# Kernel tuning notes

Hardware: AMD Instinct MI355X
Metric: run time of the kernel (lower is better)

The kernel has to match this reference:

```python
import jax, jax.numpy as jnp
import numpy as np

D_MODEL = 256
N_HEADS = 8
D_FF = 1024
N_LAYERS = 6
INPUT_DIM = 2
EPS = 1e-5  # torch LayerNorm default


def _layer_norm(x, g, b):
    m = jnp.mean(x, axis=-1, keepdims=True)
    v = jnp.mean((x - m) ** 2, axis=-1, keepdims=True)
    return (x - m) / jnp.sqrt(v + EPS) * g + b


def setup_inputs() -> dict:
    key = jax.random.key(0)
    ks = jax.random.split(key, 8)
    f32 = jnp.float32

    def w(k, shape, fan_in):
        return jax.random.normal(k, shape, f32) * (1.0 / np.sqrt(fan_in))

    return {
        "x": jax.random.normal(ks[0], (8, 1024, INPUT_DIM), f32),
        "in_w": w(ks[1], (INPUT_DIM, D_MODEL), INPUT_DIM),
        "in_b": jnp.zeros((D_MODEL,), f32),
        "ln1_g": jnp.ones((D_MODEL,), f32),
        "ln1_b": jnp.zeros((D_MODEL,), f32),
        "qkv_w": w(ks[2], (D_MODEL, 3 * D_MODEL), D_MODEL),
        "qkv_b": jnp.zeros((3 * D_MODEL,), f32),
        "out_w": w(ks[3], (D_MODEL, D_MODEL), D_MODEL),
        "out_b": jnp.zeros((D_MODEL,), f32),
        "lna_g": jnp.ones((D_MODEL,), f32),
        "lna_b": jnp.zeros((D_MODEL,), f32),
        "ln2_g": jnp.ones((D_MODEL,), f32),
        "ln2_b": jnp.zeros((D_MODEL,), f32),
        "ff1_w": w(ks[4], (D_MODEL, D_FF), D_MODEL),
        "ff1_b": jnp.zeros((D_FF,), f32),
        "ff2_w": w(ks[5], (D_FF, D_MODEL), D_FF),
        "ff2_b": jnp.zeros((D_MODEL,), f32),
        "lnf_g": jnp.ones((D_MODEL,), f32),
        "lnf_b": jnp.zeros((D_MODEL,), f32),
    }


def reference(x, in_w, in_b, ln1_g, ln1_b, qkv_w, qkv_b, out_w, out_b,
              lna_g, lna_b, ln2_g, ln2_b, ff1_w, ff1_b, ff2_w, ff2_b,
              lnf_g, lnf_b):
    B, L, _ = x.shape
    dk = D_MODEL // N_HEADS
    scale = 1.0 / np.sqrt(dk)
    top_k = max(1, L // 4)

    # sinusoidal positional encoding [L, D]
    pos = jnp.arange(L, dtype=jnp.float32)[:, None]
    div = jnp.exp(jnp.arange(0, D_MODEL, 2, dtype=jnp.float32)
                  * (-np.log(10000.0) / D_MODEL))
    pe = jnp.zeros((L, D_MODEL), jnp.float32)
    pe = pe.at[:, 0::2].set(jnp.sin(pos * div))
    pe = pe.at[:, 1::2].set(jnp.cos(pos * div))

    h = x @ in_w + in_b + pe[None]  # [B, L, D]

    # VoformerEncoder reuses the SAME layer object -> shared weights, 6 passes
    for _ in range(N_LAYERS):
        # --- self-attention sublayer (pre-norm) ---
        s2 = _layer_norm(h, ln1_g, ln1_b)
        qkv = (s2 @ qkv_w + qkv_b).reshape(B, L, 3, N_HEADS, dk)
        q = qkv[:, :, 0].transpose(0, 2, 1, 3)  # [B, H, L, dk]
        k = qkv[:, :, 1].transpose(0, 2, 1, 3)
        v = qkv[:, :, 2].transpose(0, 2, 1, 3)

        scores = jnp.einsum('bhqd,bhkd->bhqk', q, k) * scale  # [B,H,L,L]
        # ProbSparse: keep only the per-row top-k scores
        thr = jax.lax.top_k(scores, top_k)[0][..., -1:]
        sparse = jnp.where(scores >= thr, scores, -jnp.inf)
        attn = jax.nn.softmax(sparse, axis=-1)
        o = jnp.einsum('bhqk,bhkd->bhqd', attn, v)
        o = o.transpose(0, 2, 1, 3).reshape(B, L, D_MODEL)
        o = o @ out_w + out_b
        # InformerAttention applies its own residual + LayerNorm
        attn_out = _layer_norm(o + s2, lna_g, lna_b)
        h = h + attn_out

        # --- FFN sublayer with Volatilite activation ---
        s2 = _layer_norm(h, ln2_g, ln2_b)
        f = s2 @ ff1_w + ff1_b  # [B, L, d_ff]
        mean_f = jnp.mean(f, axis=1, keepdims=True)
        vol = jnp.sqrt(jnp.mean((mean_f - f) ** 2, axis=1, keepdims=True))
        f = f * vol
        f = f @ ff2_w + ff2_b
        h = h + f

    return _layer_norm(h, lnf_g, lnf_b)
```

## Files before the change

### kernel.cpp

```cpp
#include <hip/hip_runtime.h>
#include <hip/hip_bf16.h>
#include <math.h>

#define D_MODEL 256
#define NH 8
#define DFF 1024
#define NLAYERS 6
#define B_ 8
#define L_ 1024
#define NR (B_*L_)
#define TOPK 256
#define LNEPS 1e-5f

typedef __attribute__((ext_vector_type(8))) short bf16x8;
typedef __attribute__((ext_vector_type(4))) float f32x4;

__device__ __forceinline__ float wsum(float v){
  #pragma unroll
  for(int o=32;o>0;o>>=1) v += __shfl_xor(v,o,64);
  return v;
}
__device__ __forceinline__ short f2bf(float x){
  unsigned u = __float_as_uint(x);
  u += 0x7fffu + ((u>>16)&1u);
  return (short)(u>>16);
}
__device__ __forceinline__ float bf2f(short s){
  return __uint_as_float(((unsigned)(unsigned short)s)<<16);
}
__device__ __forceinline__ unsigned pk2bf(float a, float b){
  __hip_bfloat162 h = __float22bfloat162_rn(make_float2(a,b));
  unsigned u; __builtin_memcpy(&u, &h, 4);
  return u;
}
__device__ __forceinline__ float kinvf(int k){
  unsigned u = (k & 0x8000) ? ((unsigned)k ^ 0x8000u) : ((unsigned)k ^ 0xFFFFu);
  return __uint_as_float(u << 16);
}
__device__ __forceinline__ void g2l(const short* g, short* l){
  __builtin_amdgcn_global_load_lds(
      (const __attribute__((address_space(1))) unsigned int*)g,
      (__attribute__((address_space(3))) unsigned int*)l,
      16, 0, 0);
}

__global__ __launch_bounds__(256) void embed_kernel(
    const float* __restrict__ x, const float* __restrict__ in_w,
    const float* __restrict__ in_b, float* __restrict__ h)
{
  int tid = blockIdx.x*256 + threadIdx.x;
  int n  = tid >> 6;
  int d0 = (tid & 63) << 2;
  int l  = n & (L_-1);
  float x0 = x[2*n], x1 = x[2*n+1];
  const float kf = -0.07195578415606394f;
  float pe[4];
  #pragma unroll
  for(int ii=0; ii<2; ++ii){
    int i = (d0>>1) + ii;
    float dv  = expf((float)i * kf);
    float ang = (float)l * dv;
    pe[2*ii]   = sinf(ang);
    pe[2*ii+1] = cosf(ang);
  }
  float4 w0 = *(const float4*)(in_w + d0);
  float4 w1 = *(const float4*)(in_w + D_MODEL + d0);
  float4 bb = *(const float4*)(in_b + d0);
  float4 o;
  o.x = x0*w0.x + x1*w1.x + bb.x + pe[0];
  o.y = x0*w0.y + x1*w1.y + bb.y + pe[1];
  o.z = x0*w0.z + x1*w1.z + bb.z + pe[2];
  o.w = x0*w0.w + x1*w1.w + bb.w + pe[3];
  *(float4*)(h + (size_t)n*D_MODEL + d0) = o;
}

__global__ __launch_bounds__(256) void wcvt(
    const float* __restrict__ W, short* __restrict__ WT, int N, int kshift)
{
  int idx = blockIdx.x*256 + threadIdx.x;
  int K = 1<<kshift;
  if (idx >= N*K) return;
  int n = idx >> kshift, k = idx & (K-1);
  WT[idx] = f2bf(W[(size_t)k*N + n]);
}

template<int OM>
__global__ __launch_bounds__(256) void ln_kernel(
    const float* __restrict__ in, const float* __restrict__ g,
    const float* __restrict__ b, float* __restrict__ out,
    short* __restrict__ outb)
{
  int wave = threadIdx.x >> 6, lane = threadIdx.x & 63;
  int row = blockIdx.x*4 + wave;
  float4 v = ((const float4*)(in + (size_t)row*D_MODEL))[lane];
  float s  = v.x+v.y+v.z+v.w;
  float sq = v.x*v.x+v.y*v.y+v.z*v.z+v.w*v.w;
  s = wsum(s); sq = wsum(sq);
  float mean = s*(1.f/D_MODEL);
  float var  = sq*(1.f/D_MODEL) - mean*mean;
  float rstd = 1.f/sqrtf(var + LNEPS);
  float4 gv = ((const float4*)g)[lane];
  float4 bv = ((const float4*)b)[lane];
  float4 o;
  o.x = (v.x-mean)*rstd*gv.x + bv.x;
  o.y = (v.y-mean)*rstd*gv.y + bv.y;
  o.z = (v.z-mean)*rstd*gv.z + bv.z;
  o.w = (v.w-mean)*rstd*gv.w + bv.w;
  if (OM == 0){
    ((float4*)(out + (size_t)row*D_MODEL))[lane] = o;
  }
  if (OM == 2){
    uint2 pk; pk.x = pk2bf(o.x, o.y); pk.y = pk2bf(o.z, o.w);
    *(uint2*)(outb + (size_t)row*D_MODEL + lane*4) = pk;
  }
}

__global__ __launch_bounds__(256) void lnln_kernel(
    const float* __restrict__ tb,
    const float* __restrict__ ga, const float* __restrict__ ba,
    const float* __restrict__ g2, const float* __restrict__ b2,
    float* __restrict__ h, short* __restrict__ s2b)
{
  int wave = threadIdx.x >> 6, lane = threadIdx.x & 63;
  int row = blockIdx.x*4 + wave;
  float4 v = ((const float4*)(tb + (size_t)row*D_MODEL))[lane];
  float s  = v.x+v.y+v.z+v.w;
  float sq = v.x*v.x+v.y*v.y+v.z*v.z+v.w*v.w;
  s = wsum(s); sq = wsum(sq);
  float mean = s*(1.f/D_MODEL);
  float var  = sq*(1.f/D_MODEL) - mean*mean;
  float rstd = 1.f/sqrtf(var + LNEPS);
  float4 gv = ((const float4*)ga)[lane];
  float4 bv = ((const float4*)ba)[lane];
  float4* hp = (float4*)(h + (size_t)row*D_MODEL) + lane;
  float4 hv = *hp;
  float4 hn;
  hn.x = hv.x + (v.x-mean)*rstd*gv.x + bv.x;
  hn.y = hv.y + (v.y-mean)*rstd*gv.y + bv.y;
  hn.z = hv.z + (v.z-mean)*rstd*gv.z + bv.z;
  hn.w = hv.w + (v.w-mean)*rstd*gv.w + bv.w;
  *hp = hn;
  float s2  = hn.x+hn.y+hn.z+hn.w;
  float sq2 = hn.x*hn.x+hn.y*hn.y+hn.z*hn.z+hn.w*hn.w;
  s2 = wsum(s2); sq2 = wsum(sq2);
  float m2 = s2*(1.f/D_MODEL);
  float v2 = sq2*(1.f/D_MODEL) - m2*m2;
  float r2 = 1.f/sqrtf(v2 + LNEPS);
  float4 g2v = ((const float4*)g2)[lane];
  float4 b2v = ((const float4*)b2)[lane];
  uint2 pk;
  pk.x = pk2bf((hn.x-m2)*r2*g2v.x + b2v.x, (hn.y-m2)*r2*g2v.y + b2v.y);
  pk.y = pk2bf((hn.z-m2)*r2*g2v.z + b2v.z, (hn.w-m2)*r2*g2v.w + b2v.w);
  *(uint2*)(s2b + (size_t)row*D_MODEL + lane*4) = pk;
}

template<int MODE>
__global__ __launch_bounds__(256) void mfma_gemm(
    const short* __restrict__ A, const short* __restrict__ BT,
    const float* __restrict__ bias, const short* __restrict__ residb,
    float* __restrict__ Cf, short* __restrict__ Cb, short* __restrict__ Vt,
    int N, int K)
{
  __shared__ __align__(16) short As[128*32];
  __shared__ __align__(16) short Bs[64*32];
  const int t = threadIdx.x, wv = t>>6, lane = t&63;
  const int r16 = lane&15, quad = lane>>4;
  const int m0 = blockIdx.y*128, n0 = blockIdx.x*64;
  const int ia0 = wv*128 + lane, ia1 = ia0 + 64;
  const int ib  = wv*64 + lane;
  const short* Ab = A  + (size_t)m0*K;
  const short* Bb = BT + (size_t)n0*K;
  const f32x4 z = {0.f,0.f,0.f,0.f};
  f32x4 acc[2][4];
  #pragma unroll
  for (int i=0;i<2;++i)
    #pragma unroll
    for (int j=0;j<4;++j) acc[i][j] = z;

  for (int k0 = 0; k0 < K; k0 += 32){
    __syncthreads();
    g2l(Ab + (size_t)(ia0>>2)*K + k0 + (ia0&3)*8, As + ia0*8);
    g2l(Ab + (size_t)(ia1>>2)*K + k0 + (ia1&3)*8, As + ia1*8);
    g2l(Bb + (size_t)(ib>>2)*K  + k0 + (ib&3)*8,  Bs + ib*8);
    __syncthreads();
    bf16x8 af0 = *(const bf16x8*)(As + ((wv*32      + r16)*32 + quad*8));
    bf16x8 af1 = *(const bf16x8*)(As + ((wv*32 + 16 + r16)*32 + quad*8));
    bf16x8 bf[4];
    #pragma unroll
    for (int ct=0; ct<4; ++ct)
      bf[ct] = *(const bf16x8*)(Bs + ((ct*16 + r16)*32 + quad*8));
    #pragma unroll
    for (int ct=0; ct<4; ++ct){
      acc[0][ct] = __builtin_amdgcn_mfma_f32_16x16x32_bf16(af0, bf[ct], acc[0][ct], 0,0,0);
      acc[1][ct] = __builtin_amdgcn_mfma_f32_16x16x32_bf16(af1, bf[ct], acc[1][ct], 0,0,0);
    }
  }

  #pragma unroll
  for (int rt=0; rt<2; ++rt){
    const int mb = m0 + wv*32 + rt*16 + quad*4;
    #pragma unroll
    for (int ct=0; ct<4; ++ct){
      const int n = n0 + ct*16 + r16;
      const float bv = bias[n];
      if (MODE == 0){
        if (n < 512){
          int region = n>>8, hh = (n>>5)&7, d = n&31;
          #pragma unroll
          for (int r=0;r<4;++r){
            int l = mb + r;
            size_t base = (((size_t)(region*64 + (l>>10)*8 + hh))*1024 + (l&1023))*32 + d;
            Cb[base] = f2bf(acc[rt][ct][r] + bv);
          }
        } else {
          int dv = n - 512, hh = dv>>5, d = dv&31;
          int b = mb>>10, lloc = mb&1023;
          size_t base = (((size_t)(b*8 + hh))*32 + d)*1024 + lloc;
          uint2 pk;
          pk.x = pk2bf(acc[rt][ct][0] + bv, acc[rt][ct][1] + bv);
          pk.y = pk2bf(acc[rt][ct][2] + bv, acc[rt][ct][3] + bv);
          *(uint2*)(Vt + base) = pk;
        }
      } else {
        #pragma unroll
        for (int r=0;r<4;++r){
          size_t off = (size_t)(mb + r)*N + n;
          float c = acc[rt][ct][r] + bv;
          if (MODE == 1) Cf[off] = c + bf2f(residb[off]);
          if (MODE == 2) Cb[off] = f2bf(c);
          if (MODE == 3) Cf[off] += c;
        }
      }
    }
  }
}

__global__ __launch_bounds__(512,8) void attn_mfma(
    const short* __restrict__ qkbf, const short* __restrict__ vT,
    short* __restrict__ ob)
{
  __shared__ __align__(16) short sc16[16*1024];
  __shared__ __align__(16) float po[8*256];
  const int t = threadIdx.x, wv = t>>6, lane = t&63;
  const int r16 = lane&15, quad = lane>>4;
  const int blk = blockIdx.x;
  const int bh = (blk & 7)*8 + ((blk>>3)&7);
  const int qt = blk >> 6;

  bf16x8 aq = *(const bf16x8*)(qkbf + ((size_t)bh*1024 + qt*16 + r16)*32 + quad*8);
  const short* kb = qkbf + (size_t)(64 + bh)*1024*32;
  short* p0 = sc16 + quad*4096;

  #pragma unroll
  for (int g=0; g<2; ++g){
    bf16x8 bkb[4];
    #pragma unroll
    for (int j=0;j<4;++j)
      bkb[j] = *(const bf16x8*)(kb + (size_t)(wv*128 + (g*4+j)*16 + r16)*32 + quad*8);
    #pragma unroll
    for (int j=0;j<4;++j){
      f32x4 c = {0.f,0.f,0.f,0.f};
      c = __builtin_amdgcn_mfma_f32_16x16x32_bf16(aq, bkb[j], c, 0, 0, 0);
      const int keyq = (wv*128 + (g*4+j)*16 + r16) ^ ((quad&1)<<5);
      unsigned u01 = pk2bf(c[0], c[1]);
      unsigned u23 = pk2bf(c[2], c[3]);
      p0[keyq]               = (short)u01;
      p0[1024 + (keyq ^ 8)]  = (short)(u01>>16);
      p0[2048 + (keyq ^ 16)] = (short)u23;
      p0[3072 + (keyq ^ 24)] = (short)(u23>>16);
    }
  }
  __syncthreads();

  const float SC2 = 0.25500529485087056f;
  {
    const int ra = wv*2;
    const int sa = (ra&7)<<3;
    short* pa = sc16 + ra*1024 + ((2*lane) ^ sa);
    short* pb = sc16 + (ra+1)*1024 + (((2*lane) ^ sa) ^ 8);
    float fa[16], fb[16];
    #pragma unroll
    for (int i=0;i<8;++i){
      unsigned wa = *(const unsigned*)(pa + i*128);
      unsigned wb = *(const unsigned*)(pb + i*128);
      fa[2*i]   = __uint_as_float(wa << 16);
      fa[2*i+1] = __uint_as_float(wa & 0xFFFF0000u);
      fb[2*i]   = __uint_as_float(wb << 16);
      fb[2*i+1] = __uint_as_float(wb & 0xFFFF0000u);
    }
    int loA = 0, loB = 0;
    #pragma unroll
    for (int bit = 15; bit >= 0; --bit){
      const int mA = loA | (1<<bit);
      const int mB = loB | (1<<bit);
      const float tA = kinvf(mA);
      const float tB = kinvf(mB);
      int cA = 0, cB = 0;
      #pragma unroll
      for (int i=0;i<16;++i){
        cA += (int)__popcll(__ballot(fa[i] >= tA));
        cB += (int)__popcll(__ballot(fb[i] >= tB));
      }
      if (cA >= TOPK) loA = mA;
      if (cB >= TOPK) loB = mB;
    }
    const float thrA = kinvf(loA), thrB = kinvf(loB);
    float ea[16], eb[16];
    float suma = 0.f, sumb = 0.f;
    #pragma unroll
    for (int i=0;i<16;++i){
      ea[i] = (fa[i] >= thrA) ? exp2f(fa[i]*SC2) : 0.f;
      eb[i] = (fb[i] >= thrB) ? exp2f(fb[i]*SC2) : 0.f;
      suma += ea[i]; sumb += eb[i];
    }
    suma = wsum(suma); sumb = wsum(sumb);
    const float inva = 1.f/suma, invb = 1.f/sumb;
    #pragma unroll
    for (int i=0;i<8;++i){
      *(unsigned*)(pa + i*128) = pk2bf(ea[2*i]*inva, ea[2*i+1]*inva);
      *(unsigned*)(pb + i*128) = pk2bf(eb[2*i]*invb, eb[2*i+1]*invb);
    }
  }
  __syncthreads();

  const int dh = wv>>2, ks = (wv&3)*256;
  const short* vb = vT + (size_t)bh*32*1024 + (size_t)(dh*16 + r16)*1024;
  const int sA = (r16&7) << 3;
  f32x4 oa = {0.f,0.f,0.f,0.f};
  #pragma unroll
  for (int j=0;j<8;++j){
    int k0 = ks + j*32;
    bf16x8 bv = *(const bf16x8*)(vb + k0 + quad*8);
    bf16x8 af = *(const bf16x8*)(sc16 + r16*1024 + ((k0 + quad*8) ^ sA));
    oa = __builtin_amdgcn_mfma_f32_16x16x32_bf16(af, bv, oa, 0, 0, 0);
  }
  #pragma unroll
  for (int r=0;r<4;++r)
    po[wv*256 + (quad*4+r)*16 + r16] = oa[r];
  __syncthreads();
  if (t < 256){
    int q = t>>4, d = (t&15)*2;
    int h4 = (d>>4)*4;
    float v0 = 0.f, v1 = 0.f;
    #pragma unroll
    for (int w=0;w<4;++w){
      v0 += po[(h4+w)*256 + q*16 + (d&15)];
      v1 += po[(h4+w)*256 + q*16 + ((d+1)&15)];
    }
    int b = bh>>3, hh = bh&7;
    size_t off = ((size_t)(b*1024 + qt*16 + q))*256 + hh*32 + d;
    *(unsigned*)(ob + off) = pk2bf(v0, v1);
  }
}

__global__ __launch_bounds__(512) void vol_scale(short* __restrict__ f)
{
  __shared__ float ps[8][64], pq[8][64], vs[64];
  int b = blockIdx.x >> 4, cb = blockIdx.x & 15;
  int cl = threadIdx.x & 63, sl = threadIdx.x >> 6;
  int col = cb*64 + cl;
  short* fb = f + (size_t)b*L_*DFF + col;
  float s = 0.f, sq = 0.f;
  for (int l = sl*128; l < sl*128+128; ++l){
    float v = bf2f(fb[(size_t)l*DFF]);
    s += v; sq += v*v;
  }
  ps[sl][cl] = s; pq[sl][cl] = sq;
  __syncthreads();
  if (threadIdx.x < 64){
    float st=0.f, qt=0.f;
    #pragma unroll
    for (int i=0;i<8;++i){ st += ps[i][cl]; qt += pq[i][cl]; }
    float mean = st*(1.f/L_);
    float var  = qt*(1.f/L_) - mean*mean;
    vs[cl] = sqrtf(fmaxf(var, 0.f));
  }
  __syncthreads();
  float vv = vs[cl];
  for (int l = sl*128; l < sl*128+128; ++l){
    size_t o = (size_t)l*DFF;
    fb[o] = f2bf(bf2f(fb[o]) * vv);
  }
}

extern "C" void kernel_launch(void* const* d_in, const int* in_sizes, int n_in,
                              void* d_out, int out_size, void* d_ws, size_t ws_size,
                              hipStream_t stream) {
  const float* x     = (const float*)d_in[0];
  const float* in_w  = (const float*)d_in[1];
  const float* in_b  = (const float*)d_in[2];
  const float* ln1_g = (const float*)d_in[3];
  const float* ln1_b = (const float*)d_in[4];
  const float* qkv_w = (const float*)d_in[5];
  const float* qkv_b = (const float*)d_in[6];
  const float* out_w = (const float*)d_in[7];
  const float* out_b = (const float*)d_in[8];
  const float* lna_g = (const float*)d_in[9];
  const float* lna_b = (const float*)d_in[10];
  const float* ln2_g = (const float*)d_in[11];
  const float* ln2_b = (const float*)d_in[12];
  const float* ff1_w = (const float*)d_in[13];
  const float* ff1_b = (const float*)d_in[14];
  const float* ff2_w = (const float*)d_in[15];
  const float* ff2_b = (const float*)d_in[16];
  const float* lnf_g = (const float*)d_in[17];
  const float* lnf_b = (const float*)d_in[18];
  float* out = (float*)d_out;

  char* ws = (char*)d_ws;
  float* h     = (float*)(ws);
  short* s2b   = (short*)(ws + (size_t)( 8<<20));
  short* qkbf  = (short*)(ws + (size_t)(12<<20));
  short* vTb   = (short*)(ws + (size_t)(20<<20));
  short* ob_b  = (short*)(ws + (size_t)(24<<20));
  short* f     = (short*)(ws + (size_t)(12<<20));
  float* tb    = (float*)(ws + (size_t)(28<<20));
  short* qkvwT = (short*)(ws + (size_t)(36<<20));
  short* outwT = (short*)(ws + (size_t)(36<<20) + 393216);
  short* ff1wT = (short*)(ws + (size_t)(36<<20) + 393216 + 131072);
  short* ff2wT = (short*)(ws + (size_t)(36<<20) + 393216 + 131072 + 524288);

  embed_kernel<<<NR*64/256, 256, 0, stream>>>(x, in_w, in_b, h);
  wcvt<<< 768, 256, 0, stream>>>(qkv_w, qkvwT,  768, 8);
  wcvt<<< 256, 256, 0, stream>>>(out_w, outwT,  256, 8);
  wcvt<<<1024, 256, 0, stream>>>(ff1_w, ff1wT, 1024, 8);
  wcvt<<<1024, 256, 0, stream>>>(ff2_w, ff2wT,  256, 10);

  for (int layer = 0; layer < NLAYERS; ++layer){
    ln_kernel<2><<<NR/4, 256, 0, stream>>>(h, ln1_g, ln1_b, nullptr, s2b);
    {
      dim3 g(768/64, NR/128);
      mfma_gemm<0><<<g, 256, 0, stream>>>(s2b, qkvwT, qkv_b, nullptr,
                                          nullptr, qkbf, vTb, 768, 256);
    }
    attn_mfma<<<64*64, 512, 0, stream>>>(qkbf, vTb, ob_b);
    {
      dim3 g(256/64, NR/128);
      mfma_gemm<1><<<g, 256, 0, stream>>>(ob_b, outwT, out_b, s2b,
                                          tb, nullptr, nullptr, 256, 256);
    }
    lnln_kernel<<<NR/4, 256, 0, stream>>>(tb, lna_g, lna_b, ln2_g, ln2_b, h, s2b);
    {
      dim3 g(1024/64, NR/128);
      mfma_gemm<2><<<g, 256, 0, stream>>>(s2b, ff1wT, ff1_b, nullptr,
                                          nullptr, f, nullptr, 1024, 256);
    }
    vol_scale<<<B_*16, 512, 0, stream>>>(f);
    {
      dim3 g(256/64, NR/128);
      mfma_gemm<3><<<g, 256, 0, stream>>>(f, ff2wT, ff2_b, nullptr,
                                          h, nullptr, nullptr, 256, 1024);
    }
  }
  ln_kernel<0><<<NR/4, 256, 0, stream>>>(h, lnf_g, lnf_b, out, nullptr);
}
```

Before: 1.166 ms.

## Fuse volatility stats into FF1 epilogue and fold scale into per-batch FF2 weights

The FF1 GEMM epilogue now accumulates per-column sums and sums of squares into per-tile partial buffers, removing the separate vol_scale kernel that re-read and re-wrote the whole FF1 activation. A small volw2 kernel reduces these partials into per-batch volatility and writes a per-batch scaled copy of the FF2 weight, which the FF2 GEMM selects by batch. The statistics use fp32 values before bf16 rounding, and the scale is now applied in bf16 on the weights. The attention output reduction also gets an XOR-swizzled shared layout with float2 reads to reduce bank conflicts.

After: 1.170 ms. Within noise of the previous version (+0.3%).

```diff
diff --git a/kernel.cpp b/kernel.cpp
--- a/kernel.cpp
+++ b/kernel.cpp
@@ -159,6 +159,7 @@
     const short* __restrict__ A, const short* __restrict__ BT,
     const float* __restrict__ bias, const short* __restrict__ residb,
     float* __restrict__ Cf, short* __restrict__ Cb, short* __restrict__ Vt,
+    float* __restrict__ psum, float* __restrict__ psq,
     int N, int K)
 {
   __shared__ __align__(16) short As[128*32];
@@ -170,6 +171,7 @@
   const int ib  = wv*64 + lane;
   const short* Ab = A  + (size_t)m0*K;
   const short* Bb = BT + (size_t)n0*K;
+  if (MODE == 3) Bb += (size_t)(m0>>10)*262144;
   const f32x4 z = {0.f,0.f,0.f,0.f};
   f32x4 acc[2][4];
   #pragma unroll
@@ -196,6 +198,7 @@
     }
   }
 
+  float cs[4] = {0.f,0.f,0.f,0.f}, cq[4] = {0.f,0.f,0.f,0.f};
   #pragma unroll
   for (int rt=0; rt<2; ++rt){
     const int mb = m0 + wv*32 + rt*16 + quad*4;
@@ -227,12 +230,60 @@
           size_t off = (size_t)(mb + r)*N + n;
           float c = acc[rt][ct][r] + bv;
           if (MODE == 1) Cf[off] = c + bf2f(residb[off]);
-          if (MODE == 2) Cb[off] = f2bf(c);
           if (MODE == 3) Cf[off] += c;
+          if (MODE == 4){
+            Cb[off] = f2bf(c);
+            cs[ct] += c; cq[ct] += c*c;
+          }
         }
       }
     }
   }
+
+  if (MODE == 4){
+    __syncthreads();
+    float* wsm = (float*)As;
+    #pragma unroll
+    for (int ct=0; ct<4; ++ct){
+      float s = cs[ct], q = cq[ct];
+      s += __shfl_xor(s,16,64); s += __shfl_xor(s,32,64);
+      q += __shfl_xor(q,16,64); q += __shfl_xor(q,32,64);
+      if (quad == 0){
+        wsm[wv*64 + ct*16 + r16]       = s;
+        wsm[256 + wv*64 + ct*16 + r16] = q;
+      }
+    }
+    __syncthreads();
+    if (t < 64){
+      float s = wsm[t] + wsm[64+t] + wsm[128+t] + wsm[192+t];
+      psum[(size_t)blockIdx.y*1024 + n0 + t] = s;
+    } else if (t < 128){
+      int c = t - 64;
+      float q = wsm[256+c] + wsm[320+c] + wsm[384+c] + wsm[448+c];
+      psq[(size_t)blockIdx.y*1024 + n0 + c] = q;
+    }
+  }
+}
+
+__global__ __launch_bounds__(256) void volw2(
+    const float* __restrict__ psum, const float* __restrict__ psq,
+    const short* __restrict__ w2t, short* __restrict__ sw2)
+{
+  const int b = blockIdx.x>>2, kb = blockIdx.x&3;
+  const int k = kb*256 + threadIdx.x;
+  float s = 0.f, q = 0.f;
+  #pragma unroll
+  for (int m=0;m<8;++m){
+    s += psum[(size_t)(b*8+m)*1024 + k];
+    q += psq [(size_t)(b*8+m)*1024 + k];
+  }
+  float mean = s*(1.f/L_);
+  float var  = q*(1.f/L_) - mean*mean;
+  const float vol = sqrtf(fmaxf(var, 0.f));
+  short* dst = sw2 + (size_t)b*262144 + k;
+  const short* src = w2t + k;
+  for (int n=0; n<256; ++n)
+    dst[(size_t)n*1024] = f2bf(bf2f(src[(size_t)n*1024]) * vol);
 }
 
 __global__ __launch_bounds__(512,8) void attn_mfma(
@@ -335,51 +386,24 @@
     oa = __builtin_amdgcn_mfma_f32_16x16x32_bf16(af, bv, oa, 0, 0, 0);
   }
   #pragma unroll
-  for (int r=0;r<4;++r)
-    po[wv*256 + (quad*4+r)*16 + r16] = oa[r];
+  for (int r=0;r<4;++r){
+    int row = quad*4 + r;
+    po[wv*256 + ((row*16 + r16) ^ ((quad&1)<<4))] = oa[r];
+  }
   __syncthreads();
   if (t < 256){
     int q = t>>4, d = (t&15)*2;
     int h4 = (d>>4)*4;
+    int idx = (q*16 + (d&15)) ^ (((q>>2)&1)<<4);
     float v0 = 0.f, v1 = 0.f;
     #pragma unroll
     for (int w=0;w<4;++w){
-      v0 += po[(h4+w)*256 + q*16 + (d&15)];
-      v1 += po[(h4+w)*256 + q*16 + ((d+1)&15)];
+      float2 p = *(const float2*)(po + (h4+w)*256 + idx);
+      v0 += p.x; v1 += p.y;
     }
     int b = bh>>3, hh = bh&7;
     size_t off = ((size_t)(b*1024 + qt*16 + q))*256 + hh*32 + d;
     *(unsigned*)(ob + off) = pk2bf(v0, v1);
-  }
-}
-
-__global__ __launch_bounds__(512) void vol_scale(short* __restrict__ f)
-{
-  __shared__ float ps[8][64], pq[8][64], vs[64];
-  int b = blockIdx.x >> 4, cb = blockIdx.x & 15;
-  int cl = threadIdx.x & 63, sl = threadIdx.x >> 6;
-  int col = cb*64 + cl;
-  short* fb = f + (size_t)b*L_*DFF + col;
-  float s = 0.f, sq = 0.f;
-  for (int l = sl*128; l < sl*128+128; ++l){
-    float v = bf2f(fb[(size_t)l*DFF]);
-    s += v; sq += v*v;
-  }
-  ps[sl][cl] = s; pq[sl][cl] = sq;
-  __syncthreads();
-  if (threadIdx.x < 64){
-    float st=0.f, qt=0.f;
-    #pragma unroll
-    for (int i=0;i<8;++i){ st += ps[i][cl]; qt += pq[i][cl]; }
-    float mean = st*(1.f/L_);
-    float var  = qt*(1.f/L_) - mean*mean;
-    vs[cl] = sqrtf(fmaxf(var, 0.f));
-  }
-  __syncthreads();
-  float vv = vs[cl];
-  for (int l = sl*128; l < sl*128+128; ++l){
-    size_t o = (size_t)l*DFF;
-    fb[o] = f2bf(bf2f(fb[o]) * vv);
   }
 }
 
@@ -419,6 +443,9 @@
   short* outwT = (short*)(ws + (size_t)(36<<20) + 393216);
   short* ff1wT = (short*)(ws + (size_t)(36<<20) + 393216 + 131072);
   short* ff2wT = (short*)(ws + (size_t)(36<<20) + 393216 + 131072 + 524288);
+  float* psum  = (float*)(ws + (size_t)(38<<20));
+  float* psq   = (float*)(ws + (size_t)(38<<20) + 262144);
+  short* sw2   = (short*)(ws + (size_t)(38<<20) + 524288);
 
   embed_kernel<<<NR*64/256, 256, 0, stream>>>(x, in_w, in_b, h);
   wcvt<<< 768, 256, 0, stream>>>(qkv_w, qkvwT,  768, 8);
@@ -431,25 +458,29 @@
     {
       dim3 g(768/64, NR/128);
       mfma_gemm<0><<<g, 256, 0, stream>>>(s2b, qkvwT, qkv_b, nullptr,
-                                          nullptr, qkbf, vTb, 768, 256);
+                                          nullptr, qkbf, vTb, nullptr, nullptr,
+                                          768, 256);
     }
     attn_mfma<<<64*64, 512, 0, stream>>>(qkbf, vTb, ob_b);
     {
       dim3 g(256/64, NR/128);
       mfma_gemm<1><<<g, 256, 0, stream>>>(ob_b, outwT, out_b, s2b,
-                                          tb, nullptr, nullptr, 256, 256);
+                                          tb, nullptr, nullptr, nullptr, nullptr,
+                                          256, 256);
     }
     lnln_kernel<<<NR/4, 256, 0, stream>>>(tb, lna_g, lna_b, ln2_g, ln2_b, h, s2b);
     {
       dim3 g(1024/64, NR/128);
-      mfma_gemm<2><<<g, 256, 0, stream>>>(s2b, ff1wT, ff1_b, nullptr,
-                                          nullptr, f, nullptr, 1024, 256);
-    }
-    vol_scale<<<B_*16, 512, 0, stream>>>(f);
+      mfma_gemm<4><<<g, 256, 0, stream>>>(s2b, ff1wT, ff1_b, nullptr,
+                                          nullptr, f, nullptr, psum, psq,
+                                          1024, 256);
+    }
+    volw2<<<32, 256, 0, stream>>>(psum, psq, ff2wT, sw2);
     {
       dim3 g(256/64, NR/128);
-      mfma_gemm<3><<<g, 256, 0, stream>>>(f, ff2wT, ff2_b, nullptr,
-                                          h, nullptr, nullptr, 256, 1024);
+      mfma_gemm<3><<<g, 256, 0, stream>>>(f, sw2, ff2_b, nullptr,
+                                          h, nullptr, nullptr, nullptr, nullptr,
+                                          256, 1024);
     }
   }
   ln_kernel<0><<<NR/4, 256, 0, stream>>>(h, lnf_g, lnf_b, out, nullptr);
```
